# Kernel optimization log

Measured on AMD Instinct MI355X. Metric: run time of the kernel, lower is better.

The kernel has to match this reference:

```python
import jax, jax.numpy as jnp
import numpy as np


def _shared_mlp(x, W, s, b):
    # 1x1 conv over channel dim (last axis) + folded BN (scale/shift) + ReLU
    # x: (..., Cin), W: (Cout, Cin), s/b: (Cout,)
    return jax.nn.relu(jnp.einsum('...c,oc->...o', x, W) * s + b)


def setup_inputs() -> dict:
    key = jax.random.key(0)
    ks = jax.random.split(key, 15)
    B, N, K, C = 4, 4096, 32, 64
    D1, D2, DH = 64, 64, 128
    sc = 0.1
    return {
        'xyz': jax.random.normal(ks[0], (B, N, 3), dtype=jnp.float32),
        'features': jax.random.normal(ks[1], (B, C, N), dtype=jnp.float32),
        'idx': jax.random.randint(ks[2], (N, K), 0, N, dtype=jnp.int32),
        'W_gu': jax.random.normal(ks[3], (D1, 6), dtype=jnp.float32) * sc,
        's_gu': jnp.ones((D1,), jnp.float32),
        'b_gu': jax.random.normal(ks[4], (D1,), dtype=jnp.float32) * sc,
        'W_gv': jax.random.normal(ks[5], (D2, C), dtype=jnp.float32) * sc,
        's_gv': jnp.ones((D2,), jnp.float32),
        'b_gv': jax.random.normal(ks[6], (D2,), dtype=jnp.float32) * sc,
        'W_h': jax.random.normal(ks[7], (DH, D1 + D2), dtype=jnp.float32) * sc,
        's_h': jnp.ones((DH,), jnp.float32),
        'b_h': jax.random.normal(ks[8], (DH,), dtype=jnp.float32) * sc,
        'W_f': jax.random.normal(ks[9], (C, DH), dtype=jnp.float32) * sc,
        's_f': jnp.ones((C,), jnp.float32),
        'b_f': jax.random.normal(ks[10], (C,), dtype=jnp.float32) * sc,
    }


def reference(xyz, features, idx, W_gu, s_gu, b_gu, W_gv, s_gv, b_gv,
              W_h, s_h, b_h, W_f, s_f, b_f):
    # xyz: (B,N,3), features: (B,C,N), idx: (N,K) neighbor indices per point
    feats = jnp.swapaxes(features, 1, 2)              # (B,N,C)
    xyz_nb = xyz[:, idx, :]                           # (B,N,K,3) random gather
    feat_nb = feats[:, idx, :]                        # (B,N,K,C)
    K = idx.shape[1]
    center_xyz = jnp.broadcast_to(xyz[:, :, None, :], xyz_nb.shape)
    rel_xyz = jnp.concatenate([center_xyz, xyz_nb], axis=-1)   # (B,N,K,6)
    rel_feat = feat_nb + feats[:, :, None, :]                  # (B,N,K,C)

    gu = _shared_mlp(rel_xyz, W_gu, s_gu, b_gu)       # (B,N,K,D1)
    gv = _shared_mlp(rel_feat, W_gv, s_gv, b_gv)      # (B,N,K,D2)
    fuse = jnp.concatenate([gu, gv], axis=-1)         # (B,N,K,D1+D2)
    h = _shared_mlp(fuse, W_h, s_h, b_h)              # (B,N,K,DH)
    pooled = jnp.mean(h, axis=2)                      # (B,N,DH) mean over K
    out = _shared_mlp(pooled, W_f, s_f, b_f)          # (B,N,C)
    out = jnp.swapaxes(out, 1, 2) + features          # (B,C,N) residual
    return (xyz, out)
```

## Files before the change

kernel.cpp:

```cpp
#include <hip/hip_runtime.h>

#define B_  4
#define N_  4096
#define K_  32
#define C_  64
#define D1_ 64
#define D2_ 64
#define DH_ 128
#define PPB 8

typedef short  short8   __attribute__((ext_vector_type(8)));
typedef float  floatx16 __attribute__((ext_vector_type(16)));
typedef unsigned short ushort_t;
typedef unsigned int   uint_t;

__device__ __forceinline__ float bf_lo(uint_t u){ union{uint_t i;float f;} x; x.i = u << 16; return x.f; }
__device__ __forceinline__ float bf_hi(uint_t u){ union{uint_t i;float f;} x; x.i = u & 0xffff0000u; return x.f; }
__device__ __forceinline__ uint_t bf_of(float f){ union{float f;uint_t i;} x; x.f = f; uint_t b = x.i; return (b + 0x7fffu + ((b >> 16) & 1u)) >> 16; }
__device__ __forceinline__ uint_t bf_pk(float a, float b){ return bf_of(a) | (bf_of(b) << 16); }

__global__ __launch_bounds__(256) void k_transforms(
    const float* __restrict__ xyz,
    const float* __restrict__ W_gv,
    const float* __restrict__ W_h,
    const float* __restrict__ W_f,
    float* __restrict__ out_xyz,
    float* __restrict__ W_gvT,
    ushort_t* __restrict__ Bpack,
    float* __restrict__ W_fT)
{
    int e = blockIdx.x * 256 + threadIdx.x;
    if (e < B_*N_*3) { out_xyz[e] = xyz[e]; return; }
    e -= B_*N_*3;
    if (e < D2_*C_) { int o = e >> 6, c = e & 63; W_gvT[c*D2_ + o] = W_gv[e]; return; }
    e -= D2_*C_;
    if (e < DH_*(D1_+D2_)) {
        int j = e & 7, l = (e >> 3) & 63, c = (e >> 9) & 7, w = e >> 12;
        int o = w*32 + (l & 31);
        int i = c*16 + (l >> 5)*8 + j;
        Bpack[e] = (ushort_t)bf_of(W_h[o*(D1_+D2_) + i]);
        return;
    }
    e -= DH_*(D1_+D2_);
    if (e < C_*DH_) { int i = e >> 6, c = e & 63; W_fT[e] = W_f[c*DH_ + i]; }
}

__global__ __launch_bounds__(256) void k_pre(
    const float* __restrict__ xyz,
    const float* __restrict__ features,
    const float* __restrict__ W_gvT,
    const float* __restrict__ W_gu,
    const float* __restrict__ s_gu, const float* __restrict__ b_gu,
    const float* __restrict__ s_gv, const float* __restrict__ b_gv,
    float* __restrict__ Qs,
    ushort_t* __restrict__ Pcat)
{
    const int b  = blockIdx.x >> 6;
    const int n0 = (blockIdx.x & 63) * 64;
    const int t  = threadIdx.x;

    __shared__ __align__(16) float ftile[64 * 66];
    __shared__ float xs[192];
    __shared__ float wgu[384];

    const int nn = t & 63, cq = t >> 6;
#pragma unroll
    for (int r = 0; r < 16; r++) {
        int c = cq * 16 + r;
        ftile[c*66 + nn] = features[(b*C_ + c)*N_ + n0 + nn];
    }
    if (t < 192) xs[t] = xyz[(b*N_ + n0)*3 + t];
    if (t < 128) { wgu[t] = W_gu[t]; wgu[t+128] = W_gu[t+128]; wgu[t+256] = W_gu[t+256]; }
    __syncthreads();

    const int nt = t & 31, ot = t >> 5;
    const int nl0 = nt * 2, o0 = ot * 8;

    float acc[2][8] = {};
    for (int c = 0; c < 64; c++) {
        float a0 = ftile[c*66 + nl0];
        float a1 = ftile[c*66 + nl0 + 1];
        float wv[8];
        *(float4*)&wv[0] = *(const float4*)&W_gvT[c*64 + o0];
        *(float4*)&wv[4] = *(const float4*)&W_gvT[c*64 + o0 + 4];
#pragma unroll
        for (int oo = 0; oo < 8; oo++) {
            acc[0][oo] = fmaf(a0, wv[oo], acc[0][oo]);
            acc[1][oo] = fmaf(a1, wv[oo], acc[1][oo]);
        }
    }

    float sgu[8], bgu[8], sgv[8], bgv[8];
    *(float4*)&sgu[0] = *(const float4*)&s_gu[o0]; *(float4*)&sgu[4] = *(const float4*)&s_gu[o0+4];
    *(float4*)&bgu[0] = *(const float4*)&b_gu[o0]; *(float4*)&bgu[4] = *(const float4*)&b_gu[o0+4];
    *(float4*)&sgv[0] = *(const float4*)&s_gv[o0]; *(float4*)&sgv[4] = *(const float4*)&s_gv[o0+4];
    *(float4*)&bgv[0] = *(const float4*)&b_gv[o0]; *(float4*)&bgv[4] = *(const float4*)&b_gv[o0+4];

#pragma unroll
    for (int kk = 0; kk < 2; kk++) {
        const int nl = nl0 + kk;
        const int bn = b*N_ + n0 + nl;
        const float x0 = xs[nl*3], x1 = xs[nl*3+1], x2 = xs[nl*3+2];
        float qv[8], rv[8];
#pragma unroll
        for (int oo = 0; oo < 8; oo++) {
            const int o = o0 + oo;
            qv[oo] = x0*wgu[o*6+0] + x1*wgu[o*6+1] + x2*wgu[o*6+2];
            rv[oo] = x0*wgu[o*6+3] + x1*wgu[o*6+4] + x2*wgu[o*6+5];
        }
        float qs[8];
#pragma unroll
        for (int oo = 0; oo < 8; oo++) qs[oo] = qv[oo]*sgu[oo] + bgu[oo];
        *(float4*)&Qs[bn*128 + o0]     = *(float4*)&qs[0];
        *(float4*)&Qs[bn*128 + o0 + 4] = *(float4*)&qs[4];
        uint4 pk;
        pk.x = bf_pk(rv[0]*sgu[0], rv[1]*sgu[1]);
        pk.y = bf_pk(rv[2]*sgu[2], rv[3]*sgu[3]);
        pk.z = bf_pk(rv[4]*sgu[4], rv[5]*sgu[5]);
        pk.w = bf_pk(rv[6]*sgu[6], rv[7]*sgu[7]);
        *(uint4*)&Pcat[bn*128 + o0] = pk;

#pragma unroll
        for (int oo = 0; oo < 8; oo++) qs[oo] = acc[kk][oo]*sgv[oo] + bgv[oo];
        *(float4*)&Qs[bn*128 + 64 + o0]     = *(float4*)&qs[0];
        *(float4*)&Qs[bn*128 + 64 + o0 + 4] = *(float4*)&qs[4];
        pk.x = bf_pk(acc[kk][0]*sgv[0], acc[kk][1]*sgv[1]);
        pk.y = bf_pk(acc[kk][2]*sgv[2], acc[kk][3]*sgv[3]);
        pk.z = bf_pk(acc[kk][4]*sgv[4], acc[kk][5]*sgv[5]);
        pk.w = bf_pk(acc[kk][6]*sgv[6], acc[kk][7]*sgv[7]);
        *(uint4*)&Pcat[bn*128 + 64 + o0] = pk;
    }
}

__global__ __launch_bounds__(256) void k_main(
    const int*    __restrict__ idx,
    const float*  __restrict__ Qs,
    const ushort_t* __restrict__ Pcat,
    const ushort_t* __restrict__ Bpack,
    const float*  __restrict__ s_h, const float* __restrict__ b_h,
    float* __restrict__ Pool)
{
    const int t    = threadIdx.x;
    const int w    = t >> 6;
    const int lane = t & 63;
    const int m    = lane & 31;
    const int hh   = lane >> 5;

    __shared__ uint_t fuse[32 * 65];

    short8 Bf[8];
#pragma unroll
    for (int c = 0; c < 8; c++)
        Bf[c] = *(const short8*)&Bpack[((w*8 + c)*64 + lane)*8];

    const int o = w*32 + m;
    const float sh = s_h[o], bh = b_h[o];
    const int i0 = lane * 2;

    for (int p = 0; p < PPB; p++) {
        const int bn   = blockIdx.x * PPB + p;
        const int n    = bn & (N_ - 1);
        const int base = bn - n;
        const int jall = idx[n*K_ + m];
        const float2 q2 = *(const float2*)&Qs[bn*128 + i0];

        __syncthreads();
#pragma unroll
        for (int it = 0; it < 8; it++) {
            const int row = it*4 + w;
            const int j   = __shfl(jall, row);
            const uint_t rp = *(const uint_t*)&Pcat[(base + j)*128 + i0];
            const float v0 = fmaxf(q2.x + bf_lo(rp), 0.f);
            const float v1 = fmaxf(q2.y + bf_hi(rp), 0.f);
            fuse[row*65 + lane] = bf_pk(v0, v1);
        }
        __syncthreads();

        floatx16 acc = {};
#pragma unroll
        for (int c = 0; c < 8; c++) {
            const int wb = m*65 + c*8 + hh*4;
            union { uint_t u[4]; short8 s; } av;
            av.u[0] = fuse[wb+0]; av.u[1] = fuse[wb+1];
            av.u[2] = fuse[wb+2]; av.u[3] = fuse[wb+3];
            acc = __builtin_amdgcn_mfma_f32_32x32x16_bf16(av.s, Bf[c], acc, 0, 0, 0);
        }

        float v = 0.f;
#pragma unroll
        for (int r = 0; r < 16; r++)
            v += fmaxf(acc[r]*sh + bh, 0.f);
        v += __shfl_xor(v, 32);
        if (hh == 0) Pool[bn*128 + o] = v;
    }
}

__global__ __launch_bounds__(256) void k_post(
    const float* __restrict__ Pool,
    const float* __restrict__ W_fT,
    const float* __restrict__ s_f, const float* __restrict__ b_f,
    const float* __restrict__ features,
    float* __restrict__ outF)
{
    const int b   = blockIdx.x >> 6;
    const int n0  = (blockIdx.x & 63) * 64;
    const int t   = threadIdx.x;
    const int bn0 = b*N_ + n0;

    __shared__ float pt[64 * 129];

    for (int e = t; e < 64*128; e += 256) {
        int row = e >> 7, col = e & 127;
        pt[row*129 + col] = Pool[(bn0 + row)*128 + col];
    }
    __syncthreads();

    const int nt = t & 31, ct = t >> 5;
    const int nl0 = nt * 2, c0 = ct * 8;

    float acc[2][8] = {};
    for (int i = 0; i < 128; i++) {
        float p0 = pt[nl0*129 + i];
        float p1 = pt[nl0*129 + 129 + i];
        float wv[8];
        *(float4*)&wv[0] = *(const float4*)&W_fT[i*64 + c0];
        *(float4*)&wv[4] = *(const float4*)&W_fT[i*64 + c0 + 4];
#pragma unroll
        for (int oo = 0; oo < 8; oo++) {
            acc[0][oo] = fmaf(p0, wv[oo], acc[0][oo]);
            acc[1][oo] = fmaf(p1, wv[oo], acc[1][oo]);
        }
    }
    float sf[8], bfv[8];
    *(float4*)&sf[0]  = *(const float4*)&s_f[c0]; *(float4*)&sf[4]  = *(const float4*)&s_f[c0+4];
    *(float4*)&bfv[0] = *(const float4*)&b_f[c0]; *(float4*)&bfv[4] = *(const float4*)&b_f[c0+4];
#pragma unroll
    for (int oo = 0; oo < 8; oo++) {
        const int c = c0 + oo;
        const float2 fr = *(const float2*)&features[(b*C_ + c)*N_ + n0 + nl0];
        float2 ov;
        ov.x = fmaxf(acc[0][oo]*(1.f/(float)K_)*sf[oo] + bfv[oo], 0.f) + fr.x;
        ov.y = fmaxf(acc[1][oo]*(1.f/(float)K_)*sf[oo] + bfv[oo], 0.f) + fr.y;
        *(float2*)&outF[(b*C_ + c)*N_ + n0 + nl0] = ov;
    }
}

extern "C" void kernel_launch(void* const* d_in, const int* in_sizes, int n_in,
                              void* d_out, int out_size, void* d_ws, size_t ws_size,
                              hipStream_t stream)
{
    const float* xyz      = (const float*)d_in[0];
    const float* features = (const float*)d_in[1];
    const int*   idx      = (const int*)  d_in[2];
    const float* W_gu     = (const float*)d_in[3];
    const float* s_gu     = (const float*)d_in[4];
    const float* b_gu     = (const float*)d_in[5];
    const float* W_gv     = (const float*)d_in[6];
    const float* s_gv     = (const float*)d_in[7];
    const float* b_gv     = (const float*)d_in[8];
    const float* W_h      = (const float*)d_in[9];
    const float* s_h      = (const float*)d_in[10];
    const float* b_h      = (const float*)d_in[11];
    const float* W_f      = (const float*)d_in[12];
    const float* s_f      = (const float*)d_in[13];
    const float* b_f      = (const float*)d_in[14];

    float* out  = (float*)d_out;
    float* outF = out + B_*N_*3;

    char* wp = (char*)d_ws;
    float*    Qs    = (float*)wp;    wp += (size_t)B_*N_*128*4;
    float*    Pool  = (float*)wp;    wp += (size_t)B_*N_*128*4;
    ushort_t* Pcat  = (ushort_t*)wp; wp += (size_t)B_*N_*128*2;
    float*    W_gvT = (float*)wp;    wp += D2_*C_*4;
    ushort_t* Bpack = (ushort_t*)wp; wp += DH_*(D1_+D2_)*2;
    float*    W_fT  = (float*)wp;    wp += C_*DH_*4;

    k_transforms<<<304, 256, 0, stream>>>(xyz, W_gv, W_h, W_f, out, W_gvT, Bpack, W_fT);
    k_pre<<<B_*(N_/64), 256, 0, stream>>>(xyz, features, W_gvT, W_gu,
                                          s_gu, b_gu, s_gv, b_gv, Qs, Pcat);
    k_main<<<(B_*N_)/PPB, 256, 0, stream>>>(idx, Qs, Pcat, Bpack, s_h, b_h, Pool);
    k_post<<<B_*(N_/64), 256, 0, stream>>>(Pool, W_fT, s_f, b_f, features, outF);
}
```

Baseline: 145.5 us.

## Process two points per k_main round and shrink pre/post tiles for more blocks

k_main now gathers neighbor rows for two points per round, so each wave runs two MFMA accumulators over two output blocks while sharing each A fragment load. This halves the number of barrier-separated rounds per block. k_pre and k_post switch from 64-point to 16-point tiles, which quadruples the grid and uses float4 loads and stores, with an LDS transpose in k_post for coalesced output. The price is more registers in k_main (two B fragment sets) and more small blocks in the pre and post kernels.

```diff
diff --git a/kernel.cpp b/kernel.cpp
--- a/kernel.cpp
+++ b/kernel.cpp
@@ -35,8 +35,8 @@
     if (e < D2_*C_) { int o = e >> 6, c = e & 63; W_gvT[c*D2_ + o] = W_gv[e]; return; }
     e -= D2_*C_;
     if (e < DH_*(D1_+D2_)) {
-        int j = e & 7, l = (e >> 3) & 63, c = (e >> 9) & 7, w = e >> 12;
-        int o = w*32 + (l & 31);
+        int j = e & 7, l = (e >> 3) & 63, c = (e >> 9) & 7, ob = e >> 12;
+        int o = ob*32 + (l & 31);
         int i = c*16 + (l >> 5)*8 + j;
         Bpack[e] = (ushort_t)bf_of(W_h[o*(D1_+D2_) + i]);
         return;
@@ -55,89 +55,73 @@
     float* __restrict__ Qs,
     ushort_t* __restrict__ Pcat)
 {
-    const int b  = blockIdx.x >> 6;
-    const int n0 = (blockIdx.x & 63) * 64;
+    const int b  = blockIdx.x >> 8;
+    const int n0 = (blockIdx.x & 255) * 16;
     const int t  = threadIdx.x;
 
-    __shared__ __align__(16) float ftile[64 * 66];
-    __shared__ float xs[192];
-    __shared__ float wgu[384];
-
-    const int nn = t & 63, cq = t >> 6;
-#pragma unroll
-    for (int r = 0; r < 16; r++) {
-        int c = cq * 16 + r;
-        ftile[c*66 + nn] = features[(b*C_ + c)*N_ + n0 + nn];
-    }
-    if (t < 192) xs[t] = xyz[(b*N_ + n0)*3 + t];
-    if (t < 128) { wgu[t] = W_gu[t]; wgu[t+128] = W_gu[t+128]; wgu[t+256] = W_gu[t+256]; }
+    __shared__ float ftile[64 * 17];
+
+    {
+        const int c = t >> 2, nq = t & 3;
+        float4 f4 = *(const float4*)&features[(b*C_ + c)*N_ + n0 + nq*4];
+        ftile[c*17 + nq*4 + 0] = f4.x;
+        ftile[c*17 + nq*4 + 1] = f4.y;
+        ftile[c*17 + nq*4 + 2] = f4.z;
+        ftile[c*17 + nq*4 + 3] = f4.w;
+    }
     __syncthreads();
 
-    const int nt = t & 31, ot = t >> 5;
-    const int nl0 = nt * 2, o0 = ot * 8;
-
-    float acc[2][8] = {};
+    const int n  = t >> 4;
+    const int oq = t & 15;
+    const int o0 = oq * 4;
+
+    float acc[4] = {};
     for (int c = 0; c < 64; c++) {
-        float a0 = ftile[c*66 + nl0];
-        float a1 = ftile[c*66 + nl0 + 1];
-        float wv[8];
-        *(float4*)&wv[0] = *(const float4*)&W_gvT[c*64 + o0];
-        *(float4*)&wv[4] = *(const float4*)&W_gvT[c*64 + o0 + 4];
-#pragma unroll
-        for (int oo = 0; oo < 8; oo++) {
-            acc[0][oo] = fmaf(a0, wv[oo], acc[0][oo]);
-            acc[1][oo] = fmaf(a1, wv[oo], acc[1][oo]);
-        }
-    }
-
-    float sgu[8], bgu[8], sgv[8], bgv[8];
-    *(float4*)&sgu[0] = *(const float4*)&s_gu[o0]; *(float4*)&sgu[4] = *(const float4*)&s_gu[o0+4];
-    *(float4*)&bgu[0] = *(const float4*)&b_gu[o0]; *(float4*)&bgu[4] = *(const float4*)&b_gu[o0+4];
-    *(float4*)&sgv[0] = *(const float4*)&s_gv[o0]; *(float4*)&sgv[4] = *(const float4*)&s_gv[o0+4];
-    *(float4*)&bgv[0] = *(const float4*)&b_gv[o0]; *(float4*)&bgv[4] = *(const float4*)&b_gv[o0+4];
-
-#pragma unroll
-    for (int kk = 0; kk < 2; kk++) {
-        const int nl = nl0 + kk;
-        const int bn = b*N_ + n0 + nl;
-        const float x0 = xs[nl*3], x1 = xs[nl*3+1], x2 = xs[nl*3+2];
-        float qv[8], rv[8];
-#pragma unroll
-        for (int oo = 0; oo < 8; oo++) {
-            const int o = o0 + oo;
-            qv[oo] = x0*wgu[o*6+0] + x1*wgu[o*6+1] + x2*wgu[o*6+2];
-            rv[oo] = x0*wgu[o*6+3] + x1*wgu[o*6+4] + x2*wgu[o*6+5];
-        }
-        float qs[8];
-#pragma unroll
-        for (int oo = 0; oo < 8; oo++) qs[oo] = qv[oo]*sgu[oo] + bgu[oo];
-        *(float4*)&Qs[bn*128 + o0]     = *(float4*)&qs[0];
-        *(float4*)&Qs[bn*128 + o0 + 4] = *(float4*)&qs[4];
-        uint4 pk;
-        pk.x = bf_pk(rv[0]*sgu[0], rv[1]*sgu[1]);
-        pk.y = bf_pk(rv[2]*sgu[2], rv[3]*sgu[3]);
-        pk.z = bf_pk(rv[4]*sgu[4], rv[5]*sgu[5]);
-        pk.w = bf_pk(rv[6]*sgu[6], rv[7]*sgu[7]);
-        *(uint4*)&Pcat[bn*128 + o0] = pk;
-
-#pragma unroll
-        for (int oo = 0; oo < 8; oo++) qs[oo] = acc[kk][oo]*sgv[oo] + bgv[oo];
-        *(float4*)&Qs[bn*128 + 64 + o0]     = *(float4*)&qs[0];
-        *(float4*)&Qs[bn*128 + 64 + o0 + 4] = *(float4*)&qs[4];
-        pk.x = bf_pk(acc[kk][0]*sgv[0], acc[kk][1]*sgv[1]);
-        pk.y = bf_pk(acc[kk][2]*sgv[2], acc[kk][3]*sgv[3]);
-        pk.z = bf_pk(acc[kk][4]*sgv[4], acc[kk][5]*sgv[5]);
-        pk.w = bf_pk(acc[kk][6]*sgv[6], acc[kk][7]*sgv[7]);
-        *(uint4*)&Pcat[bn*128 + 64 + o0] = pk;
-    }
+        const float a = ftile[c*17 + n];
+        const float4 wv = *(const float4*)&W_gvT[c*64 + o0];
+        acc[0] = fmaf(a, wv.x, acc[0]);
+        acc[1] = fmaf(a, wv.y, acc[1]);
+        acc[2] = fmaf(a, wv.z, acc[2]);
+        acc[3] = fmaf(a, wv.w, acc[3]);
+    }
+
+    const int bn = b*N_ + n0 + n;
+    const float x0 = xyz[bn*3+0], x1 = xyz[bn*3+1], x2 = xyz[bn*3+2];
+
+    const float4 sgu = *(const float4*)&s_gu[o0];
+    const float4 bgu = *(const float4*)&b_gu[o0];
+    const float4 sgv = *(const float4*)&s_gv[o0];
+    const float4 bgv = *(const float4*)&b_gv[o0];
+
+    float q[4], r[4];
+#pragma unroll
+    for (int j = 0; j < 4; j++) {
+        const int o = o0 + j;
+        q[j] = x0*W_gu[o*6+0] + x1*W_gu[o*6+1] + x2*W_gu[o*6+2];
+        r[j] = x0*W_gu[o*6+3] + x1*W_gu[o*6+4] + x2*W_gu[o*6+5];
+    }
+    float4 qs;
+    qs.x = q[0]*sgu.x + bgu.x; qs.y = q[1]*sgu.y + bgu.y;
+    qs.z = q[2]*sgu.z + bgu.z; qs.w = q[3]*sgu.w + bgu.w;
+    *(float4*)&Qs[bn*128 + o0] = qs;
+    uint2 pk;
+    pk.x = bf_pk(r[0]*sgu.x, r[1]*sgu.y);
+    pk.y = bf_pk(r[2]*sgu.z, r[3]*sgu.w);
+    *(uint2*)&Pcat[bn*128 + o0] = pk;
+    qs.x = acc[0]*sgv.x + bgv.x; qs.y = acc[1]*sgv.y + bgv.y;
+    qs.z = acc[2]*sgv.z + bgv.z; qs.w = acc[3]*sgv.w + bgv.w;
+    *(float4*)&Qs[bn*128 + 64 + o0] = qs;
+    pk.x = bf_pk(acc[0]*sgv.x, acc[1]*sgv.y);
+    pk.y = bf_pk(acc[2]*sgv.z, acc[3]*sgv.w);
+    *(uint2*)&Pcat[bn*128 + 64 + o0] = pk;
 }
 
 __global__ __launch_bounds__(256) void k_main(
-    const int*    __restrict__ idx,
-    const float*  __restrict__ Qs,
+    const int*      __restrict__ idx,
+    const float*    __restrict__ Qs,
     const ushort_t* __restrict__ Pcat,
     const ushort_t* __restrict__ Bpack,
-    const float*  __restrict__ s_h, const float* __restrict__ b_h,
+    const float*    __restrict__ s_h, const float* __restrict__ b_h,
     float* __restrict__ Pool)
 {
     const int t    = threadIdx.x;
@@ -145,53 +129,72 @@
     const int lane = t & 63;
     const int m    = lane & 31;
     const int hh   = lane >> 5;
-
-    __shared__ uint_t fuse[32 * 65];
-
-    short8 Bf[8];
-#pragma unroll
-    for (int c = 0; c < 8; c++)
-        Bf[c] = *(const short8*)&Bpack[((w*8 + c)*64 + lane)*8];
-
-    const int o = w*32 + m;
-    const float sh = s_h[o], bh = b_h[o];
-    const int i0 = lane * 2;
-
-    for (int p = 0; p < PPB; p++) {
-        const int bn   = blockIdx.x * PPB + p;
-        const int n    = bn & (N_ - 1);
-        const int base = bn - n;
-        const int jall = idx[n*K_ + m];
-        const float2 q2 = *(const float2*)&Qs[bn*128 + i0];
+    const int slot = w >> 1;
+    const int oh   = w & 1;
+
+    __shared__ uint_t fuse[2 * 32 * 66];
+
+    short8 Bf[2][8];
+#pragma unroll
+    for (int ob = 0; ob < 2; ob++)
+#pragma unroll
+        for (int c = 0; c < 8; c++)
+            Bf[ob][c] = *(const short8*)&Bpack[(((oh*2 + ob)*8 + c)*64 + lane)*8];
+
+    float sh[2], bh[2];
+#pragma unroll
+    for (int ob = 0; ob < 2; ob++) {
+        sh[ob] = s_h[(oh*2 + ob)*32 + m];
+        bh[ob] = b_h[(oh*2 + ob)*32 + m];
+    }
+
+    for (int rr = 0; rr < PPB/2; rr++) {
+        const int bn0   = blockIdx.x * PPB + rr*2;
+        const int base0 = bn0 & ~(N_ - 1);
+
+        const int jall = idx[((bn0 + hh) & (N_-1))*K_ + m];
+        float2 q2[2];
+        q2[0] = *(const float2*)&Qs[(bn0+0)*128 + lane*2];
+        q2[1] = *(const float2*)&Qs[(bn0+1)*128 + lane*2];
 
         __syncthreads();
 #pragma unroll
-        for (int it = 0; it < 8; it++) {
-            const int row = it*4 + w;
-            const int j   = __shfl(jall, row);
-            const uint_t rp = *(const uint_t*)&Pcat[(base + j)*128 + i0];
-            const float v0 = fmaxf(q2.x + bf_lo(rp), 0.f);
-            const float v1 = fmaxf(q2.y + bf_hi(rp), 0.f);
-            fuse[row*65 + lane] = bf_pk(v0, v1);
+        for (int it = 0; it < 16; it++) {
+            const int rs  = it*4 + w;
+            const int sl  = rs >> 5, row = rs & 31;
+            const int j   = __shfl(jall, rs);
+            const uint_t rp = *(const uint_t*)&Pcat[(base0 + j)*128 + lane*2];
+            const float2 q  = q2[sl];
+            const float v0 = fmaxf(q.x + bf_lo(rp), 0.f);
+            const float v1 = fmaxf(q.y + bf_hi(rp), 0.f);
+            fuse[sl*2112 + row*66 + lane] = bf_pk(v0, v1);
         }
         __syncthreads();
 
-        floatx16 acc = {};
+        floatx16 acc0 = {}, acc1 = {};
 #pragma unroll
         for (int c = 0; c < 8; c++) {
-            const int wb = m*65 + c*8 + hh*4;
+            const int wb = slot*2112 + m*66 + c*8 + hh*4;
             union { uint_t u[4]; short8 s; } av;
-            av.u[0] = fuse[wb+0]; av.u[1] = fuse[wb+1];
-            av.u[2] = fuse[wb+2]; av.u[3] = fuse[wb+3];
-            acc = __builtin_amdgcn_mfma_f32_32x32x16_bf16(av.s, Bf[c], acc, 0, 0, 0);
-        }
-
-        float v = 0.f;
-#pragma unroll
-        for (int r = 0; r < 16; r++)
-            v += fmaxf(acc[r]*sh + bh, 0.f);
-        v += __shfl_xor(v, 32);
-        if (hh == 0) Pool[bn*128 + o] = v;
+            *(uint2*)&av.u[0] = *(const uint2*)&fuse[wb];
+            *(uint2*)&av.u[2] = *(const uint2*)&fuse[wb + 2];
+            acc0 = __builtin_amdgcn_mfma_f32_32x32x16_bf16(av.s, Bf[0][c], acc0, 0, 0, 0);
+            acc1 = __builtin_amdgcn_mfma_f32_32x32x16_bf16(av.s, Bf[1][c], acc1, 0, 0, 0);
+        }
+
+        const int bnp = bn0 + slot;
+        float v0 = 0.f, v1 = 0.f;
+#pragma unroll
+        for (int rg = 0; rg < 16; rg++) {
+            v0 += fmaxf(acc0[rg]*sh[0] + bh[0], 0.f);
+            v1 += fmaxf(acc1[rg]*sh[1] + bh[1], 0.f);
+        }
+        v0 += __shfl_xor(v0, 32);
+        v1 += __shfl_xor(v1, 32);
+        if (hh == 0) {
+            Pool[bnp*128 + (oh*2+0)*32 + m] = v0;
+            Pool[bnp*128 + (oh*2+1)*32 + m] = v1;
+        }
     }
 }
 
@@ -202,46 +205,54 @@
     const float* __restrict__ features,
     float* __restrict__ outF)
 {
-    const int b   = blockIdx.x >> 6;
-    const int n0  = (blockIdx.x & 63) * 64;
+    const int b   = blockIdx.x >> 8;
+    const int n0  = (blockIdx.x & 255) * 16;
     const int t   = threadIdx.x;
     const int bn0 = b*N_ + n0;
 
-    __shared__ float pt[64 * 129];
-
-    for (int e = t; e < 64*128; e += 256) {
-        int row = e >> 7, col = e & 127;
-        pt[row*129 + col] = Pool[(bn0 + row)*128 + col];
+    __shared__ float pt[16 * 132];
+    __shared__ float ot[64 * 17];
+
+    {
+        const int n = t >> 4, iq = t & 15;
+        float4 p0 = *(const float4*)&Pool[(bn0 + n)*128 + iq*8];
+        float4 p1 = *(const float4*)&Pool[(bn0 + n)*128 + iq*8 + 4];
+        *(float4*)&pt[n*132 + iq*8]     = p0;
+        *(float4*)&pt[n*132 + iq*8 + 4] = p1;
     }
     __syncthreads();
 
-    const int nt = t & 31, ct = t >> 5;
-    const int nl0 = nt * 2, c0 = ct * 8;
-
-    float acc[2][8] = {};
+    const int n  = t >> 4;
+    const int cq = t & 15;
+    const int c0 = cq * 4;
+
+    float acc[4] = {};
     for (int i = 0; i < 128; i++) {
-        float p0 = pt[nl0*129 + i];
-        float p1 = pt[nl0*129 + 129 + i];
-        float wv[8];
-        *(float4*)&wv[0] = *(const float4*)&W_fT[i*64 + c0];
-        *(float4*)&wv[4] = *(const float4*)&W_fT[i*64 + c0 + 4];
-#pragma unroll
-        for (int oo = 0; oo < 8; oo++) {
-            acc[0][oo] = fmaf(p0, wv[oo], acc[0][oo]);
-            acc[1][oo] = fmaf(p1, wv[oo], acc[1][oo]);
-        }
-    }
-    float sf[8], bfv[8];
-    *(float4*)&sf[0]  = *(const float4*)&s_f[c0]; *(float4*)&sf[4]  = *(const float4*)&s_f[c0+4];
-    *(float4*)&bfv[0] = *(const float4*)&b_f[c0]; *(float4*)&bfv[4] = *(const float4*)&b_f[c0+4];
-#pragma unroll
-    for (int oo = 0; oo < 8; oo++) {
-        const int c = c0 + oo;
-        const float2 fr = *(const float2*)&features[(b*C_ + c)*N_ + n0 + nl0];
-        float2 ov;
-        ov.x = fmaxf(acc[0][oo]*(1.f/(float)K_)*sf[oo] + bfv[oo], 0.f) + fr.x;
-        ov.y = fmaxf(acc[1][oo]*(1.f/(float)K_)*sf[oo] + bfv[oo], 0.f) + fr.y;
-        *(float2*)&outF[(b*C_ + c)*N_ + n0 + nl0] = ov;
+        const float p = pt[n*132 + i];
+        const float4 wv = *(const float4*)&W_fT[i*64 + c0];
+        acc[0] = fmaf(p, wv.x, acc[0]);
+        acc[1] = fmaf(p, wv.y, acc[1]);
+        acc[2] = fmaf(p, wv.z, acc[2]);
+        acc[3] = fmaf(p, wv.w, acc[3]);
+    }
+    const float4 sf = *(const float4*)&s_f[c0];
+    const float4 bf = *(const float4*)&b_f[c0];
+    const float inv_k = 1.f / (float)K_;
+    ot[(c0+0)*17 + n] = fmaxf(acc[0]*inv_k*sf.x + bf.x, 0.f);
+    ot[(c0+1)*17 + n] = fmaxf(acc[1]*inv_k*sf.y + bf.y, 0.f);
+    ot[(c0+2)*17 + n] = fmaxf(acc[2]*inv_k*sf.z + bf.z, 0.f);
+    ot[(c0+3)*17 + n] = fmaxf(acc[3]*inv_k*sf.w + bf.w, 0.f);
+    __syncthreads();
+
+    {
+        const int c = t >> 2, nq = t & 3;
+        const float4 fr = *(const float4*)&features[(b*C_ + c)*N_ + n0 + nq*4];
+        float4 ov;
+        ov.x = ot[c*17 + nq*4 + 0] + fr.x;
+        ov.y = ot[c*17 + nq*4 + 1] + fr.y;
+        ov.z = ot[c*17 + nq*4 + 2] + fr.z;
+        ov.w = ot[c*17 + nq*4 + 3] + fr.w;
+        *(float4*)&outF[(b*C_ + c)*N_ + n0 + nq*4] = ov;
     }
 }
 
@@ -277,8 +288,8 @@
     float*    W_fT  = (float*)wp;    wp += C_*DH_*4;
 
     k_transforms<<<304, 256, 0, stream>>>(xyz, W_gv, W_h, W_f, out, W_gvT, Bpack, W_fT);
-    k_pre<<<B_*(N_/64), 256, 0, stream>>>(xyz, features, W_gvT, W_gu,
+    k_pre<<<B_*(N_/16), 256, 0, stream>>>(xyz, features, W_gvT, W_gu,
                                           s_gu, b_gu, s_gv, b_gv, Qs, Pcat);
     k_main<<<(B_*N_)/PPB, 256, 0, stream>>>(idx, Qs, Pcat, Bpack, s_h, b_h, Pool);
-    k_post<<<B_*(N_/64), 256, 0, stream>>>(Pool, W_fT, s_f, b_f, features, outF);
-}
+    k_post<<<B_*(N_/16), 256, 0, stream>>>(Pool, W_fT, s_f, b_f, features, outF);
+}
```

Result: slower. 172.0 us (+18.2%).
